# Kernel tuning notes

Measured on AMD Instinct MI355X. Metric: run time of the kernel, lower is better.

The kernel has to match this reference:

```python
import jax, jax.numpy as jnp
import numpy as np
import math

B, C, T = 32, 512, 1024
QUERY_DIM = 512
SCALE = 1.0 / math.sqrt(QUERY_DIM)


def setup_inputs() -> dict:
    key = jax.random.key(0)
    ks = jax.random.split(key, 10)
    lim = 1.0 / math.sqrt(C)  # torch Linear default init range
    return {
        "x": jax.random.normal(ks[0], (B, C, T), dtype=jnp.float32),
        "g_query": jax.random.uniform(ks[1], (B, C, T), dtype=jnp.float32),
        "g_keys": jax.random.uniform(ks[2], (B, C, T), dtype=jnp.float32),
        "g_values": jax.random.uniform(ks[3], (B, C, T), dtype=jnp.float32),
        "Wq": jax.random.uniform(ks[4], (C, C), jnp.float32, -lim, lim),
        "bq": jax.random.uniform(ks[5], (C,), jnp.float32, -lim, lim),
        "Wk": jax.random.uniform(ks[6], (C, C), jnp.float32, -lim, lim),
        "bk": jax.random.uniform(ks[7], (C,), jnp.float32, -lim, lim),
        "Wv": jax.random.uniform(ks[8], (C, C), jnp.float32, -lim, lim),
        "bv": jax.random.uniform(ks[9], (C,), jnp.float32, -lim, lim),
    }


def reference(x, g_query, g_keys, g_values, Wq, bq, Wk, bk, Wv, bv):
    # x, gates: [B, C, T] -> transpose to [B, T, C]
    xt = jnp.swapaxes(x, 1, 2)
    gq = jnp.swapaxes(g_query, 1, 2)
    gk = jnp.swapaxes(g_keys, 1, 2)
    gv = jnp.swapaxes(g_values, 1, 2)
    # torch Linear: y = x @ W^T + b
    q = gq * (jnp.einsum('btc,dc->btd', xt, Wq) + bq)  # [B, T, C]
    k = gk * (jnp.einsum('btc,dc->btd', xt, Wk) + bk)  # [B, T, C]
    v = gv * (jnp.einsum('btc,dc->btd', xt, Wv) + bv)  # [B, T, C]
    # energy[b,c,d] = sum_t q[b,t,c] * k[b,t,d]  (channel-channel attention)
    energy = jnp.einsum('btc,btd->bcd', q, k)  # [B, C, C]
    attn = jax.nn.softmax(energy * SCALE, axis=2)
    # out[b,c,t] = sum_d attn[b,c,d] * v[b,t,d]
    out = jnp.einsum('bcd,btd->bct', attn, v)  # [B, C, T]
    return out
```

## Files before the change

kernel.cpp:

```cpp
#include <hip/hip_runtime.h>
#include <math.h>


#define B_ 32
#define C_ 512
#define T_ 1024
#define TC_ ((size_t)524288)
#define CC_ ((size_t)262144)
#define SCALE_ 0.04419417382415922f

typedef short bf16x8 __attribute__((ext_vector_type(8)));
typedef float f32x4 __attribute__((ext_vector_type(4)));

__device__ __forceinline__ unsigned short f2b(float f) {
    unsigned int u = __float_as_uint(f);
    u += 0x7fff + ((u >> 16) & 1);
    return (unsigned short)(u >> 16);
}
__device__ __forceinline__ float b2f(unsigned short h) {
    return __uint_as_float(((unsigned int)h) << 16);
}

#define GLDS(gp, lp) __builtin_amdgcn_global_load_lds( \
    (const __attribute__((address_space(1))) unsigned int*)(const void*)(gp), \
    (__attribute__((address_space(3))) unsigned int*)(void*)(lp), 16, 0, 0)

template<int M, int N, int K, int EP>
__global__ __launch_bounds__(256, 2) void gemm_nt(
    const unsigned short* __restrict__ Ahi, const unsigned short* __restrict__ Alo, size_t sA,
    const unsigned short* __restrict__ Bhi, const unsigned short* __restrict__ Blo, size_t sB,
    float* __restrict__ Cf, size_t sCf,
    unsigned short* __restrict__ Chi, unsigned short* __restrict__ Clo, size_t sC,
    const float* __restrict__ gate, size_t sG,
    const float* __restrict__ bias)
{
    __shared__ __attribute__((aligned(16))) unsigned short sAh[128 * 32];
    __shared__ __attribute__((aligned(16))) unsigned short sAl[128 * 32];
    __shared__ __attribute__((aligned(16))) unsigned short sBh[128 * 32];
    __shared__ __attribute__((aligned(16))) unsigned short sBl[128 * 32];

    const int tid  = threadIdx.x;
    const int lane = tid & 63;
    const int wave = tid >> 6;
    const int bz   = blockIdx.z;
    const int m0   = blockIdx.y * 128;
    const int n0   = blockIdx.x * 128;

    const unsigned short* pAh = Ahi + (size_t)bz * sA;
    const unsigned short* pAl = Alo + (size_t)bz * sA;
    const unsigned short* pBh = Bhi + (size_t)bz * sB;
    const unsigned short* pBl = Blo + (size_t)bz * sB;

    const int srow = wave * 32;
    const int lr   = lane >> 2;
    const int lk   = (lane & 3) * 8;
    const size_t gA0 = (size_t)(m0 + srow + lr) * K + lk;
    const size_t gA1 = (size_t)(m0 + srow + 16 + lr) * K + lk;
    const size_t gB0 = (size_t)(n0 + srow + lr) * K + lk;
    const size_t gB1 = (size_t)(n0 + srow + 16 + lr) * K + lk;
    unsigned short* lds0 = nullptr;  (void)lds0;

    const int wm = (wave & 1) * 64;
    const int wn = (wave >> 1) * 64;
    const int fr = lane & 15;
    const int fk = (lane >> 4) * 8;

    f32x4 acc[4][4] = {};

    for (int k0 = 0; k0 < K; k0 += 32) {
        GLDS(pAh + gA0 + k0, &sAh[srow * 32]);
        GLDS(pAh + gA1 + k0, &sAh[(srow + 16) * 32]);
        GLDS(pAl + gA0 + k0, &sAl[srow * 32]);
        GLDS(pAl + gA1 + k0, &sAl[(srow + 16) * 32]);
        GLDS(pBh + gB0 + k0, &sBh[srow * 32]);
        GLDS(pBh + gB1 + k0, &sBh[(srow + 16) * 32]);
        GLDS(pBl + gB0 + k0, &sBl[srow * 32]);
        GLDS(pBl + gB1 + k0, &sBl[(srow + 16) * 32]);
        __syncthreads();

        bf16x8 aH[4], aL[4], bH[4], bL[4];
        #pragma unroll
        for (int i = 0; i < 4; ++i) {
            int ar = (wm + i * 16 + fr) * 32 + fk;
            int br = (wn + i * 16 + fr) * 32 + fk;
            aH[i] = *(const bf16x8*)(const void*)&sAh[ar];
            aL[i] = *(const bf16x8*)(const void*)&sAl[ar];
            bH[i] = *(const bf16x8*)(const void*)&sBh[br];
            bL[i] = *(const bf16x8*)(const void*)&sBl[br];
        }
        #pragma unroll
        for (int mi = 0; mi < 4; ++mi)
            #pragma unroll
            for (int ni = 0; ni < 4; ++ni) {
                acc[mi][ni] = __builtin_amdgcn_mfma_f32_16x16x32_bf16(aL[mi], bH[ni], acc[mi][ni], 0, 0, 0);
                acc[mi][ni] = __builtin_amdgcn_mfma_f32_16x16x32_bf16(aH[mi], bL[ni], acc[mi][ni], 0, 0, 0);
                acc[mi][ni] = __builtin_amdgcn_mfma_f32_16x16x32_bf16(aH[mi], bH[ni], acc[mi][ni], 0, 0, 0);
            }
        __syncthreads();
    }

    #pragma unroll
    for (int mi = 0; mi < 4; ++mi) {
        #pragma unroll
        for (int r = 0; r < 4; ++r) {
            int m = m0 + wm + mi * 16 + (lane >> 4) * 4 + r;
            #pragma unroll
            for (int ni = 0; ni < 4; ++ni) {
                int n = n0 + wn + ni * 16 + fr;
                float v = acc[mi][ni][r];
                size_t idx = (size_t)m * N + n;
                if (EP == 0 || EP == 1) {
                    float g = gate[(size_t)bz * sG + idx];
                    float val = g * (v + bias[EP == 0 ? m : n]);
                    unsigned short h = f2b(val);
                    Chi[(size_t)bz * sC + idx] = h;
                    Clo[(size_t)bz * sC + idx] = f2b(val - b2f(h));
                } else if (EP == 2) {
                    Cf[(size_t)bz * sCf + idx] = v * SCALE_;
                } else {
                    Cf[(size_t)bz * sCf + idx] = v;
                }
            }
        }
    }
}

__global__ __launch_bounds__(256) void transpose_split(
    const float* __restrict__ x, const float* __restrict__ gv,
    unsigned short* __restrict__ xThi, unsigned short* __restrict__ xTlo,
    float* __restrict__ gvT, int bc, int b_off)
{
    __shared__ float s[64][65];
    const int z = blockIdx.z;
    const int job = z / bc, bz = z % bc;
    const int t0 = blockIdx.x * 64, c0 = blockIdx.y * 64;
    const float* src = (job ? gv : x) + (size_t)(b_off + bz) * TC_;
    const int col = threadIdx.x & 63, rb = threadIdx.x >> 6;

    #pragma unroll
    for (int i = 0; i < 64; i += 4)
        s[i + rb][col] = src[(size_t)(c0 + i + rb) * T_ + t0 + col];
    __syncthreads();

    const size_t ob = (size_t)bz * TC_;
    #pragma unroll
    for (int i = 0; i < 64; i += 4) {
        int tr = i + rb;
        float v = s[col][tr];
        size_t o = ob + (size_t)(t0 + tr) * C_ + c0 + col;
        if (job == 0) {
            unsigned short h = f2b(v);
            xThi[o] = h;
            xTlo[o] = f2b(v - b2f(h));
        } else {
            gvT[o] = v;
        }
    }
}

__global__ __launch_bounds__(256) void split_mat(
    const float* __restrict__ W, unsigned short* __restrict__ hi,
    unsigned short* __restrict__ lo, int n)
{
    int i = blockIdx.x * 256 + threadIdx.x;
    if (i < n) {
        float v = W[i];
        unsigned short h = f2b(v);
        hi[i] = h;
        lo[i] = f2b(v - b2f(h));
    }
}

__global__ __launch_bounds__(256) void softmax_split(
    const float* __restrict__ E, unsigned short* __restrict__ Ahi,
    unsigned short* __restrict__ Alo)
{
    const int row = blockIdx.x;
    const float* p = E + (size_t)row * C_;
    const int tid = threadIdx.x;

    float v0 = p[tid], v1 = p[tid + 256];
    float m = fmaxf(v0, v1);
    #pragma unroll
    for (int off = 32; off > 0; off >>= 1)
        m = fmaxf(m, __shfl_down(m, off, 64));

    __shared__ float sm[4];
    if ((tid & 63) == 0) sm[tid >> 6] = m;
    __syncthreads();
    float M = fmaxf(fmaxf(sm[0], sm[1]), fmaxf(sm[2], sm[3]));

    float e0 = expf(v0 - M), e1 = expf(v1 - M);
    float s = e0 + e1;
    #pragma unroll
    for (int off = 32; off > 0; off >>= 1)
        s += __shfl_down(s, off, 64);

    __shared__ float ss[4];
    if ((tid & 63) == 0) ss[tid >> 6] = s;
    __syncthreads();
    float inv = 1.0f / (ss[0] + ss[1] + ss[2] + ss[3]);

    float a0 = e0 * inv, a1 = e1 * inv;
    size_t o = (size_t)row * C_ + tid;
    unsigned short h0 = f2b(a0);
    Ahi[o] = h0;  Alo[o] = f2b(a0 - b2f(h0));
    unsigned short h1 = f2b(a1);
    Ahi[o + 256] = h1;  Alo[o + 256] = f2b(a1 - b2f(h1));
}

extern "C" void kernel_launch(void* const* d_in, const int* in_sizes, int n_in,
                              void* d_out, int out_size, void* d_ws, size_t ws_size,
                              hipStream_t stream) {
    const float* x  = (const float*)d_in[0];
    const float* gq = (const float*)d_in[1];
    const float* gk = (const float*)d_in[2];
    const float* gv = (const float*)d_in[3];
    const float* Wq = (const float*)d_in[4];
    const float* bq = (const float*)d_in[5];
    const float* Wk = (const float*)d_in[6];
    const float* bk = (const float*)d_in[7];
    const float* Wv = (const float*)d_in[8];
    const float* bv = (const float*)d_in[9];
    float* out = (float*)d_out;

    const size_t wBytes = 6 * CC_ * 2;
    const size_t perBatch = 2 * TC_ * 2 + TC_ * 4 + 6 * TC_ * 2
                          + CC_ * 4 + 2 * CC_ * 2;
    int bc = 1;
    for (int cand = B_; cand >= 1; cand >>= 1)
        if (wBytes + (size_t)cand * perBatch <= ws_size) { bc = cand; break; }

    char* p = (char*)d_ws;
    auto take = [&](size_t bytes) { char* r = p; p += bytes; return r; };
    unsigned short* Wqh = (unsigned short*)take(CC_ * 2);
    unsigned short* Wql = (unsigned short*)take(CC_ * 2);
    unsigned short* Wkh = (unsigned short*)take(CC_ * 2);
    unsigned short* Wkl = (unsigned short*)take(CC_ * 2);
    unsigned short* Wvh = (unsigned short*)take(CC_ * 2);
    unsigned short* Wvl = (unsigned short*)take(CC_ * 2);
    unsigned short* xThi = (unsigned short*)take((size_t)bc * TC_ * 2);
    unsigned short* xTlo = (unsigned short*)take((size_t)bc * TC_ * 2);
    float*          gvT  = (float*)take((size_t)bc * TC_ * 4);
    unsigned short* Qh = (unsigned short*)take((size_t)bc * TC_ * 2);
    unsigned short* Ql = (unsigned short*)take((size_t)bc * TC_ * 2);
    unsigned short* Kh = (unsigned short*)take((size_t)bc * TC_ * 2);
    unsigned short* Kl = (unsigned short*)take((size_t)bc * TC_ * 2);
    unsigned short* Vh = (unsigned short*)take((size_t)bc * TC_ * 2);
    unsigned short* Vl = (unsigned short*)take((size_t)bc * TC_ * 2);
    float*          E  = (float*)take((size_t)bc * CC_ * 4);
    unsigned short* Ah = (unsigned short*)take((size_t)bc * CC_ * 2);
    unsigned short* Al = (unsigned short*)take((size_t)bc * CC_ * 2);

    dim3 blk(256);
    split_mat<<<(int)(CC_ / 256), blk, 0, stream>>>(Wq, Wqh, Wql, (int)CC_);
    split_mat<<<(int)(CC_ / 256), blk, 0, stream>>>(Wk, Wkh, Wkl, (int)CC_);
    split_mat<<<(int)(CC_ / 256), blk, 0, stream>>>(Wv, Wvh, Wvl, (int)CC_);

    for (int b_off = 0; b_off < B_; b_off += bc) {
        transpose_split<<<dim3(T_ / 64, C_ / 64, 2 * bc), blk, 0, stream>>>(
            x, gv, xThi, xTlo, gvT, bc, b_off);

        gemm_nt<512, 1024, 512, 0><<<dim3(8, 4, bc), blk, 0, stream>>>(
            Wqh, Wql, 0, xThi, xTlo, TC_, nullptr, 0, Qh, Ql, TC_,
            gq + (size_t)b_off * TC_, TC_, bq);
        gemm_nt<512, 1024, 512, 0><<<dim3(8, 4, bc), blk, 0, stream>>>(
            Wkh, Wkl, 0, xThi, xTlo, TC_, nullptr, 0, Kh, Kl, TC_,
            gk + (size_t)b_off * TC_, TC_, bk);
        gemm_nt<1024, 512, 512, 1><<<dim3(4, 8, bc), blk, 0, stream>>>(
            xThi, xTlo, TC_, Wvh, Wvl, 0, nullptr, 0, Vh, Vl, TC_,
            gvT, TC_, bv);
        gemm_nt<512, 512, 1024, 2><<<dim3(4, 4, bc), blk, 0, stream>>>(
            Qh, Ql, TC_, Kh, Kl, TC_, E, CC_, nullptr, nullptr, 0, nullptr, 0, nullptr);
        softmax_split<<<dim3(bc * C_), blk, 0, stream>>>(E, Ah, Al);
        gemm_nt<512, 1024, 512, 3><<<dim3(8, 4, bc), blk, 0, stream>>>(
            Ah, Al, CC_, Vh, Vl, TC_, out + (size_t)b_off * TC_, TC_,
            nullptr, nullptr, 0, nullptr, 0, nullptr);
    }
}
```

Measured before the change: 671.1 us.

## Fuse QKV projections into one GEMM, shrink tiles, transpose V afterward

Concatenates Wq/Wk/Wv into one split weight and runs a single QKV GEMM producing V in channel-major layout. V is then transposed in bf16 hi/lo form instead of transposing the fp32 gate beforehand. The energy and output GEMMs drop to 64x64 tiles with higher occupancy hints for more blocks per batch chunk. This cuts launches and the fp32 gate-transpose traffic, but adds a bf16 transpose pass, and smaller tiles mean less operand reuse.

```diff
diff --git a/kernel.cpp b/kernel.cpp
--- a/kernel.cpp
+++ b/kernel.cpp
@@ -11,13 +11,14 @@
 
 typedef short bf16x8 __attribute__((ext_vector_type(8)));
 typedef float f32x4 __attribute__((ext_vector_type(4)));
-
-__device__ __forceinline__ unsigned short f2b(float f) {
+typedef unsigned short u16;
+
+__device__ __forceinline__ u16 f2b(float f) {
     unsigned int u = __float_as_uint(f);
     u += 0x7fff + ((u >> 16) & 1);
-    return (unsigned short)(u >> 16);
-}
-__device__ __forceinline__ float b2f(unsigned short h) {
+    return (u16)(u >> 16);
+}
+__device__ __forceinline__ float b2f(u16 h) {
     return __uint_as_float(((unsigned int)h) << 16);
 }
 
@@ -25,116 +26,186 @@
     (const __attribute__((address_space(1))) unsigned int*)(const void*)(gp), \
     (__attribute__((address_space(3))) unsigned int*)(void*)(lp), 16, 0, 0)
 
-template<int M, int N, int K, int EP>
-__global__ __launch_bounds__(256, 2) void gemm_nt(
-    const unsigned short* __restrict__ Ahi, const unsigned short* __restrict__ Alo, size_t sA,
-    const unsigned short* __restrict__ Bhi, const unsigned short* __restrict__ Blo, size_t sB,
-    float* __restrict__ Cf, size_t sCf,
-    unsigned short* __restrict__ Chi, unsigned short* __restrict__ Clo, size_t sC,
-    const float* __restrict__ gate, size_t sG,
-    const float* __restrict__ bias)
-{
-    __shared__ __attribute__((aligned(16))) unsigned short sAh[128 * 32];
-    __shared__ __attribute__((aligned(16))) unsigned short sAl[128 * 32];
-    __shared__ __attribute__((aligned(16))) unsigned short sBh[128 * 32];
-    __shared__ __attribute__((aligned(16))) unsigned short sBl[128 * 32];
+template<int TM>
+__device__ __forceinline__ void gemm_core(
+    const u16* __restrict__ Ah, const u16* __restrict__ Al,
+    const u16* __restrict__ Bh, const u16* __restrict__ Bl,
+    int m0, int n0, int kk, f32x4 (*acc)[2])
+{
+    constexpr int AM  = TM / 32;
+    constexpr int NI  = (TM / 16 + 4) * 2;
+    constexpr int NPI = NI / 4;
+    __shared__ __attribute__((aligned(16))) u16 sAh[TM * 32];
+    __shared__ __attribute__((aligned(16))) u16 sAl[TM * 32];
+    __shared__ __attribute__((aligned(16))) u16 sBh[64 * 32];
+    __shared__ __attribute__((aligned(16))) u16 sBl[64 * 32];
 
     const int tid  = threadIdx.x;
     const int lane = tid & 63;
     const int wave = tid >> 6;
-    const int bz   = blockIdx.z;
-    const int m0   = blockIdx.y * 128;
-    const int n0   = blockIdx.x * 128;
-
-    const unsigned short* pAh = Ahi + (size_t)bz * sA;
-    const unsigned short* pAl = Alo + (size_t)bz * sA;
-    const unsigned short* pBh = Bhi + (size_t)bz * sB;
-    const unsigned short* pBl = Blo + (size_t)bz * sB;
-
-    const int srow = wave * 32;
-    const int lr   = lane >> 2;
-    const int lk   = (lane & 3) * 8;
-    const size_t gA0 = (size_t)(m0 + srow + lr) * K + lk;
-    const size_t gA1 = (size_t)(m0 + srow + 16 + lr) * K + lk;
-    const size_t gB0 = (size_t)(n0 + srow + lr) * K + lk;
-    const size_t gB1 = (size_t)(n0 + srow + 16 + lr) * K + lk;
-    unsigned short* lds0 = nullptr;  (void)lds0;
-
-    const int wm = (wave & 1) * 64;
-    const int wn = (wave >> 1) * 64;
+    const int lr = lane >> 2;
+    const int lk = (lane & 3) * 8;
+    const int wm = (wave & 1) * (TM / 2);
+    const int wn = (wave >> 1) * 32;
     const int fr = lane & 15;
     const int fk = (lane >> 4) * 8;
 
-    f32x4 acc[4][4] = {};
-
-    for (int k0 = 0; k0 < K; k0 += 32) {
-        GLDS(pAh + gA0 + k0, &sAh[srow * 32]);
-        GLDS(pAh + gA1 + k0, &sAh[(srow + 16) * 32]);
-        GLDS(pAl + gA0 + k0, &sAl[srow * 32]);
-        GLDS(pAl + gA1 + k0, &sAl[(srow + 16) * 32]);
-        GLDS(pBh + gB0 + k0, &sBh[srow * 32]);
-        GLDS(pBh + gB1 + k0, &sBh[(srow + 16) * 32]);
-        GLDS(pBl + gB0 + k0, &sBl[srow * 32]);
-        GLDS(pBl + gB1 + k0, &sBl[(srow + 16) * 32]);
+    const u16* gb[NPI];
+    u16* lb[NPI];
+    #pragma unroll
+    for (int j = 0; j < NPI; ++j) {
+        int i = wave + j * 4;
+        int plane = i & 1, p = i >> 1;
+        if (p < TM / 16) {
+            gb[j] = (plane ? Al : Ah) + (size_t)(m0 + p * 16 + lr) * kk + lk;
+            lb[j] = (plane ? sAl : sAh) + p * 512;
+        } else {
+            int q = p - TM / 16;
+            gb[j] = (plane ? Bl : Bh) + (size_t)(n0 + q * 16 + lr) * kk + lk;
+            lb[j] = (plane ? sBl : sBh) + q * 512;
+        }
+    }
+
+    for (int k0 = 0; k0 < kk; k0 += 32) {
+        #pragma unroll
+        for (int j = 0; j < NPI; ++j) GLDS(gb[j] + k0, lb[j]);
         __syncthreads();
 
-        bf16x8 aH[4], aL[4], bH[4], bL[4];
-        #pragma unroll
-        for (int i = 0; i < 4; ++i) {
-            int ar = (wm + i * 16 + fr) * 32 + fk;
-            int br = (wn + i * 16 + fr) * 32 + fk;
-            aH[i] = *(const bf16x8*)(const void*)&sAh[ar];
-            aL[i] = *(const bf16x8*)(const void*)&sAl[ar];
-            bH[i] = *(const bf16x8*)(const void*)&sBh[br];
-            bL[i] = *(const bf16x8*)(const void*)&sBl[br];
-        }
-        #pragma unroll
-        for (int mi = 0; mi < 4; ++mi)
+        bf16x8 aH[AM], aL[AM], bH[2], bL[2];
+        #pragma unroll
+        for (int i = 0; i < AM; ++i) {
+            int off = (wm + i * 16 + fr) * 32 + fk;
+            aH[i] = *(const bf16x8*)(const void*)&sAh[off];
+            aL[i] = *(const bf16x8*)(const void*)&sAl[off];
+        }
+        #pragma unroll
+        for (int j = 0; j < 2; ++j) {
+            int off = (wn + j * 16 + fr) * 32 + fk;
+            bH[j] = *(const bf16x8*)(const void*)&sBh[off];
+            bL[j] = *(const bf16x8*)(const void*)&sBl[off];
+        }
+        #pragma unroll
+        for (int mi = 0; mi < AM; ++mi)
             #pragma unroll
-            for (int ni = 0; ni < 4; ++ni) {
+            for (int ni = 0; ni < 2; ++ni) {
                 acc[mi][ni] = __builtin_amdgcn_mfma_f32_16x16x32_bf16(aL[mi], bH[ni], acc[mi][ni], 0, 0, 0);
                 acc[mi][ni] = __builtin_amdgcn_mfma_f32_16x16x32_bf16(aH[mi], bL[ni], acc[mi][ni], 0, 0, 0);
                 acc[mi][ni] = __builtin_amdgcn_mfma_f32_16x16x32_bf16(aH[mi], bH[ni], acc[mi][ni], 0, 0, 0);
             }
         __syncthreads();
     }
-
-    #pragma unroll
-    for (int mi = 0; mi < 4; ++mi) {
+}
+
+__global__ __launch_bounds__(256, 3) void gemm_qkv(
+    const u16* __restrict__ Wh, const u16* __restrict__ Wl,
+    const u16* __restrict__ xTh, const u16* __restrict__ xTl,
+    const float* __restrict__ gq, const float* __restrict__ gk, const float* __restrict__ gv,
+    const float* __restrict__ bq, const float* __restrict__ bk, const float* __restrict__ bv,
+    u16* __restrict__ Qh, u16* __restrict__ Ql,
+    u16* __restrict__ Kh, u16* __restrict__ Kl,
+    u16* __restrict__ Th, u16* __restrict__ Tl)
+{
+    const int bz = blockIdx.z;
+    const int m0 = blockIdx.y * 128;
+    const int n0 = blockIdx.x * 64;
+
+    f32x4 acc[4][2] = {};
+    gemm_core<128>(Wh, Wl, xTh + (size_t)bz * TC_, xTl + (size_t)bz * TC_,
+                   m0, n0, 512, acc);
+
+    const int seg = m0 >> 9;
+    const float* gate = (seg == 0 ? gq : seg == 1 ? gk : gv) + (size_t)bz * TC_;
+    const float* bias = (seg == 0 ? bq : seg == 1 ? bk : bv);
+    u16* oh = (seg == 0 ? Qh : seg == 1 ? Kh : Th) + (size_t)bz * TC_;
+    u16* ol = (seg == 0 ? Ql : seg == 1 ? Kl : Tl) + (size_t)bz * TC_;
+
+    const int lane = threadIdx.x & 63, wave = threadIdx.x >> 6;
+    const int wm = (wave & 1) * 64, wn = (wave >> 1) * 32, fr = lane & 15;
+    #pragma unroll
+    for (int mi = 0; mi < 4; ++mi)
         #pragma unroll
         for (int r = 0; r < 4; ++r) {
-            int m = m0 + wm + mi * 16 + (lane >> 4) * 4 + r;
+            int m = (m0 & 511) + wm + mi * 16 + ((lane >> 4) << 2) + r;
+            float bb = bias[m];
             #pragma unroll
-            for (int ni = 0; ni < 4; ++ni) {
+            for (int ni = 0; ni < 2; ++ni) {
                 int n = n0 + wn + ni * 16 + fr;
-                float v = acc[mi][ni][r];
-                size_t idx = (size_t)m * N + n;
-                if (EP == 0 || EP == 1) {
-                    float g = gate[(size_t)bz * sG + idx];
-                    float val = g * (v + bias[EP == 0 ? m : n]);
-                    unsigned short h = f2b(val);
-                    Chi[(size_t)bz * sC + idx] = h;
-                    Clo[(size_t)bz * sC + idx] = f2b(val - b2f(h));
-                } else if (EP == 2) {
-                    Cf[(size_t)bz * sCf + idx] = v * SCALE_;
-                } else {
-                    Cf[(size_t)bz * sCf + idx] = v;
-                }
+                size_t idx = (size_t)m * T_ + n;
+                float val = gate[idx] * (acc[mi][ni][r] + bb);
+                u16 h = f2b(val);
+                oh[idx] = h;
+                ol[idx] = f2b(val - b2f(h));
             }
         }
-    }
+}
+
+__global__ __launch_bounds__(256, 4) void gemm_e(
+    const u16* __restrict__ Qh, const u16* __restrict__ Ql,
+    const u16* __restrict__ Kh, const u16* __restrict__ Kl,
+    float* __restrict__ E)
+{
+    const int bz = blockIdx.z;
+    const int m0 = blockIdx.y * 64;
+    const int n0 = blockIdx.x * 64;
+
+    f32x4 acc[2][2] = {};
+    gemm_core<64>(Qh + (size_t)bz * TC_, Ql + (size_t)bz * TC_,
+                  Kh + (size_t)bz * TC_, Kl + (size_t)bz * TC_,
+                  m0, n0, 1024, acc);
+
+    float* Eb = E + (size_t)bz * CC_;
+    const int lane = threadIdx.x & 63, wave = threadIdx.x >> 6;
+    const int wm = (wave & 1) * 32, wn = (wave >> 1) * 32, fr = lane & 15;
+    #pragma unroll
+    for (int mi = 0; mi < 2; ++mi)
+        #pragma unroll
+        for (int r = 0; r < 4; ++r) {
+            int m = m0 + wm + mi * 16 + ((lane >> 4) << 2) + r;
+            #pragma unroll
+            for (int ni = 0; ni < 2; ++ni) {
+                int n = n0 + wn + ni * 16 + fr;
+                Eb[(size_t)m * C_ + n] = acc[mi][ni][r] * SCALE_;
+            }
+        }
+}
+
+__global__ __launch_bounds__(256, 4) void gemm_out(
+    const u16* __restrict__ Ah, const u16* __restrict__ Al,
+    const u16* __restrict__ Vh, const u16* __restrict__ Vl,
+    float* __restrict__ out)
+{
+    const int bz = blockIdx.z;
+    const int m0 = blockIdx.y * 64;
+    const int n0 = blockIdx.x * 64;
+
+    f32x4 acc[2][2] = {};
+    gemm_core<64>(Ah + (size_t)bz * CC_, Al + (size_t)bz * CC_,
+                  Vh + (size_t)bz * TC_, Vl + (size_t)bz * TC_,
+                  m0, n0, 512, acc);
+
+    float* ob = out + (size_t)bz * TC_;
+    const int lane = threadIdx.x & 63, wave = threadIdx.x >> 6;
+    const int wm = (wave & 1) * 32, wn = (wave >> 1) * 32, fr = lane & 15;
+    #pragma unroll
+    for (int mi = 0; mi < 2; ++mi)
+        #pragma unroll
+        for (int r = 0; r < 4; ++r) {
+            int m = m0 + wm + mi * 16 + ((lane >> 4) << 2) + r;
+            #pragma unroll
+            for (int ni = 0; ni < 2; ++ni) {
+                int n = n0 + wn + ni * 16 + fr;
+                ob[(size_t)m * T_ + n] = acc[mi][ni][r];
+            }
+        }
 }
 
 __global__ __launch_bounds__(256) void transpose_split(
-    const float* __restrict__ x, const float* __restrict__ gv,
-    unsigned short* __restrict__ xThi, unsigned short* __restrict__ xTlo,
-    float* __restrict__ gvT, int bc, int b_off)
+    const float* __restrict__ x, u16* __restrict__ xThi, u16* __restrict__ xTlo)
 {
     __shared__ float s[64][65];
-    const int z = blockIdx.z;
-    const int job = z / bc, bz = z % bc;
+    const int bz = blockIdx.z;
     const int t0 = blockIdx.x * 64, c0 = blockIdx.y * 64;
-    const float* src = (job ? gv : x) + (size_t)(b_off + bz) * TC_;
+    const float* src = x + (size_t)bz * TC_;
     const int col = threadIdx.x & 63, rb = threadIdx.x >> 6;
 
     #pragma unroll
@@ -148,32 +219,58 @@
         int tr = i + rb;
         float v = s[col][tr];
         size_t o = ob + (size_t)(t0 + tr) * C_ + c0 + col;
-        if (job == 0) {
-            unsigned short h = f2b(v);
-            xThi[o] = h;
-            xTlo[o] = f2b(v - b2f(h));
-        } else {
-            gvT[o] = v;
-        }
-    }
-}
-
-__global__ __launch_bounds__(256) void split_mat(
-    const float* __restrict__ W, unsigned short* __restrict__ hi,
-    unsigned short* __restrict__ lo, int n)
-{
-    int i = blockIdx.x * 256 + threadIdx.x;
-    if (i < n) {
-        float v = W[i];
-        unsigned short h = f2b(v);
-        hi[i] = h;
-        lo[i] = f2b(v - b2f(h));
-    }
+        u16 h = f2b(v);
+        xThi[o] = h;
+        xTlo[o] = f2b(v - b2f(h));
+    }
+}
+
+__global__ __launch_bounds__(256) void transpose_bf(
+    const u16* __restrict__ s0, const u16* __restrict__ s1,
+    u16* __restrict__ d0p, u16* __restrict__ d1p, int bc)
+{
+    __shared__ u16 s[64][65];
+    const int z = blockIdx.z;
+    const int plane = z >= bc ? 1 : 0;
+    const int bz = z - plane * bc;
+    const u16* src = (plane ? s1 : s0) + (size_t)bz * TC_;
+    u16* dst = (plane ? d1p : d0p) + (size_t)bz * TC_;
+    const int d0 = blockIdx.y * 64, t0 = blockIdx.x * 64;
+    const int tp = threadIdx.x & 31, rr = threadIdx.x >> 5;
+
+    #pragma unroll
+    for (int i = 0; i < 64; i += 8) {
+        int d = i + rr;
+        ushort2 v = *(const ushort2*)(const void*)&src[(size_t)(d0 + d) * T_ + t0 + tp * 2];
+        s[tp * 2][d] = v.x;
+        s[tp * 2 + 1][d] = v.y;
+    }
+    __syncthreads();
+    #pragma unroll
+    for (int i = 0; i < 64; i += 8) {
+        int t = i + rr;
+        ushort2 v;
+        v.x = s[t][tp * 2];
+        v.y = s[t][tp * 2 + 1];
+        *(ushort2*)(void*)&dst[(size_t)(t0 + t) * C_ + d0 + tp * 2] = v;
+    }
+}
+
+__global__ __launch_bounds__(256) void split_w(
+    const float* __restrict__ Wq, const float* __restrict__ Wk,
+    const float* __restrict__ Wv, u16* __restrict__ hi, u16* __restrict__ lo)
+{
+    size_t i = (size_t)blockIdx.x * 256 + threadIdx.x;
+    const float* src = i < CC_ ? Wq : (i < 2 * CC_ ? Wk : Wv);
+    size_t off = i < CC_ ? i : (i < 2 * CC_ ? i - CC_ : i - 2 * CC_);
+    float v = src[off];
+    u16 h = f2b(v);
+    hi[i] = h;
+    lo[i] = f2b(v - b2f(h));
 }
 
 __global__ __launch_bounds__(256) void softmax_split(
-    const float* __restrict__ E, unsigned short* __restrict__ Ahi,
-    unsigned short* __restrict__ Alo)
+    const float* __restrict__ E, u16* __restrict__ Ahi, u16* __restrict__ Alo)
 {
     const int row = blockIdx.x;
     const float* p = E + (size_t)row * C_;
@@ -203,9 +300,9 @@
 
     float a0 = e0 * inv, a1 = e1 * inv;
     size_t o = (size_t)row * C_ + tid;
-    unsigned short h0 = f2b(a0);
+    u16 h0 = f2b(a0);
     Ahi[o] = h0;  Alo[o] = f2b(a0 - b2f(h0));
-    unsigned short h1 = f2b(a1);
+    u16 h1 = f2b(a1);
     Ahi[o + 256] = h1;  Alo[o + 256] = f2b(a1 - b2f(h1));
 }
 
@@ -224,57 +321,44 @@
     const float* bv = (const float*)d_in[9];
     float* out = (float*)d_out;
 
-    const size_t wBytes = 6 * CC_ * 2;
-    const size_t perBatch = 2 * TC_ * 2 + TC_ * 4 + 6 * TC_ * 2
-                          + CC_ * 4 + 2 * CC_ * 2;
+    const size_t wBytes = 2 * (3 * CC_) * 2;
+    const size_t perBatch = 10 * TC_ * 2 + CC_ * 4 + 2 * CC_ * 2;
     int bc = 1;
     for (int cand = B_; cand >= 1; cand >>= 1)
         if (wBytes + (size_t)cand * perBatch <= ws_size) { bc = cand; break; }
 
     char* p = (char*)d_ws;
     auto take = [&](size_t bytes) { char* r = p; p += bytes; return r; };
-    unsigned short* Wqh = (unsigned short*)take(CC_ * 2);
-    unsigned short* Wql = (unsigned short*)take(CC_ * 2);
-    unsigned short* Wkh = (unsigned short*)take(CC_ * 2);
-    unsigned short* Wkl = (unsigned short*)take(CC_ * 2);
-    unsigned short* Wvh = (unsigned short*)take(CC_ * 2);
-    unsigned short* Wvl = (unsigned short*)take(CC_ * 2);
-    unsigned short* xThi = (unsigned short*)take((size_t)bc * TC_ * 2);
-    unsigned short* xTlo = (unsigned short*)take((size_t)bc * TC_ * 2);
-    float*          gvT  = (float*)take((size_t)bc * TC_ * 4);
-    unsigned short* Qh = (unsigned short*)take((size_t)bc * TC_ * 2);
-    unsigned short* Ql = (unsigned short*)take((size_t)bc * TC_ * 2);
-    unsigned short* Kh = (unsigned short*)take((size_t)bc * TC_ * 2);
-    unsigned short* Kl = (unsigned short*)take((size_t)bc * TC_ * 2);
-    unsigned short* Vh = (unsigned short*)take((size_t)bc * TC_ * 2);
-    unsigned short* Vl = (unsigned short*)take((size_t)bc * TC_ * 2);
-    float*          E  = (float*)take((size_t)bc * CC_ * 4);
-    unsigned short* Ah = (unsigned short*)take((size_t)bc * CC_ * 2);
-    unsigned short* Al = (unsigned short*)take((size_t)bc * CC_ * 2);
+    u16* Wh  = (u16*)take(3 * CC_ * 2);
+    u16* Wl  = (u16*)take(3 * CC_ * 2);
+    u16* xTh = (u16*)take((size_t)bc * TC_ * 2);
+    u16* xTl = (u16*)take((size_t)bc * TC_ * 2);
+    u16* Qh  = (u16*)take((size_t)bc * TC_ * 2);
+    u16* Ql  = (u16*)take((size_t)bc * TC_ * 2);
+    u16* Kh  = (u16*)take((size_t)bc * TC_ * 2);
+    u16* Kl  = (u16*)take((size_t)bc * TC_ * 2);
+    u16* Th  = (u16*)take((size_t)bc * TC_ * 2);
+    u16* Tl  = (u16*)take((size_t)bc * TC_ * 2);
+    u16* Vh  = (u16*)take((size_t)bc * TC_ * 2);
+    u16* Vl  = (u16*)take((size_t)bc * TC_ * 2);
+    float* E = (float*)take((size_t)bc * CC_ * 4);
+    u16* Ah  = (u16*)take((size_t)bc * CC_ * 2);
+    u16* Al  = (u16*)take((size_t)bc * CC_ * 2);
 
     dim3 blk(256);
-    split_mat<<<(int)(CC_ / 256), blk, 0, stream>>>(Wq, Wqh, Wql, (int)CC_);
-    split_mat<<<(int)(CC_ / 256), blk, 0, stream>>>(Wk, Wkh, Wkl, (int)CC_);
-    split_mat<<<(int)(CC_ / 256), blk, 0, stream>>>(Wv, Wvh, Wvl, (int)CC_);
+    split_w<<<(int)(3 * CC_ / 256), blk, 0, stream>>>(Wq, Wk, Wv, Wh, Wl);
 
     for (int b_off = 0; b_off < B_; b_off += bc) {
-        transpose_split<<<dim3(T_ / 64, C_ / 64, 2 * bc), blk, 0, stream>>>(
-            x, gv, xThi, xTlo, gvT, bc, b_off);
-
-        gemm_nt<512, 1024, 512, 0><<<dim3(8, 4, bc), blk, 0, stream>>>(
-            Wqh, Wql, 0, xThi, xTlo, TC_, nullptr, 0, Qh, Ql, TC_,
-            gq + (size_t)b_off * TC_, TC_, bq);
-        gemm_nt<512, 1024, 512, 0><<<dim3(8, 4, bc), blk, 0, stream>>>(
-            Wkh, Wkl, 0, xThi, xTlo, TC_, nullptr, 0, Kh, Kl, TC_,
-            gk + (size_t)b_off * TC_, TC_, bk);
-        gemm_nt<1024, 512, 512, 1><<<dim3(4, 8, bc), blk, 0, stream>>>(
-            xThi, xTlo, TC_, Wvh, Wvl, 0, nullptr, 0, Vh, Vl, TC_,
-            gvT, TC_, bv);
-        gemm_nt<512, 512, 1024, 2><<<dim3(4, 4, bc), blk, 0, stream>>>(
-            Qh, Ql, TC_, Kh, Kl, TC_, E, CC_, nullptr, nullptr, 0, nullptr, 0, nullptr);
+        transpose_split<<<dim3(16, 8, bc), blk, 0, stream>>>(
+            x + (size_t)b_off * TC_, xTh, xTl);
+        gemm_qkv<<<dim3(16, 12, bc), blk, 0, stream>>>(
+            Wh, Wl, xTh, xTl,
+            gq + (size_t)b_off * TC_, gk + (size_t)b_off * TC_, gv + (size_t)b_off * TC_,
+            bq, bk, bv, Qh, Ql, Kh, Kl, Th, Tl);
+        transpose_bf<<<dim3(16, 8, 2 * bc), blk, 0, stream>>>(Th, Tl, Vh, Vl, bc);
+        gemm_e<<<dim3(8, 8, bc), blk, 0, stream>>>(Qh, Ql, Kh, Kl, E);
         softmax_split<<<dim3(bc * C_), blk, 0, stream>>>(E, Ah, Al);
-        gemm_nt<512, 1024, 512, 3><<<dim3(8, 4, bc), blk, 0, stream>>>(
-            Ah, Al, CC_, Vh, Vl, TC_, out + (size_t)b_off * TC_, TC_,
-            nullptr, nullptr, 0, nullptr, 0, nullptr);
-    }
-}
+        gemm_out<<<dim3(16, 8, bc), blk, 0, stream>>>(
+            Ah, Al, Vh, Vl, out + (size_t)b_off * TC_);
+    }
+}
```

Result: slower. 732.7 us (+9.2%).
